# Kernel optimization log

Hardware: AMD Instinct MI355X
Metric: run time of the kernel (lower is better)

## Reference

```python
import jax, jax.numpy as jnp
import numpy as np

B, DIM, L, H, W = 4, 128, 256, 8, 8
N = L * H * W
D_INNER, D_STATE, D_CONV, DT_RANK = 128, 8, 4, 8


def _ln(x, w, b, eps=1e-5):
    m = x.mean(-1, keepdims=True)
    v = ((x - m) ** 2).mean(-1, keepdims=True)
    return (x - m) * jax.lax.rsqrt(v + eps) * w + b


def _mamba_fusion(x, z_in, p, i):
    # x, z_in: (B, N, DIM). x drives the SSM; z_in provides the cross-modal gate.
    u = x @ p['Wx'][i]                                    # (B, N, D_INNER)
    z = z_in @ p['Wz'][i]                                 # (B, N, D_INNER)
    # causal depthwise conv1d along tokens, kernel D_CONV (torch pad=k-1 then truncate)
    up = jnp.pad(u, ((0, 0), (D_CONV - 1, 0), (0, 0)))
    w = p['conv_w'][i]                                    # (D_INNER, D_CONV)
    uc = sum(up[:, k:k + u.shape[1], :] * w[:, k] for k in range(D_CONV)) + p['conv_b'][i]
    uc = jax.nn.silu(uc)
    x_dbl = uc @ p['Wxproj'][i]                           # (B, N, DT_RANK + 2*D_STATE)
    dt_r, Bm, Cm = jnp.split(x_dbl, [DT_RANK, DT_RANK + D_STATE], axis=-1)
    dt = jax.nn.softplus(dt_r @ p['Wdt'][i] + p['bdt'][i])  # (B, N, D_INNER)
    A = -jnp.exp(p['A_log'][i])                           # (D_INNER, D_STATE)
    dA = jnp.exp(dt[..., None] * A)                       # (B, N, D_INNER, D_STATE)
    dBu = dt[..., None] * Bm[:, :, None, :] * uc[..., None]

    def step(h, inp):
        dA_t, dBu_t, C_t = inp
        h = dA_t * h + dBu_t                              # (B, D_INNER, D_STATE)
        return h, jnp.einsum('bds,bs->bd', h, C_t)

    h0 = jnp.zeros((u.shape[0], D_INNER, D_STATE), u.dtype)
    _, ys = jax.lax.scan(step, h0, (dA.swapaxes(0, 1), dBu.swapaxes(0, 1), Cm.swapaxes(0, 1)))
    y = ys.swapaxes(0, 1) + p['Dp'][i] * uc
    y = y * jax.nn.silu(z)
    return y @ p['Wout_m'][i] + p['bout_m'][i]


def _cross_block(in0, in1, p, i):
    skip = in0
    a = _ln(in0, p['ln0_w'][i], p['ln0_b'][i])
    b = _ln(in1, p['ln1_w'][i], p['ln1_b'][i])
    return skip + _mamba_fusion(a, b, p, i)


def setup_inputs() -> dict:
    key = jax.random.key(0)
    ks = jax.random.split(key, 16)
    s_in = 1.0 / np.sqrt(DIM)
    s_di = 1.0 / np.sqrt(D_INNER)
    inp = {
        'front': jax.random.normal(ks[0], (B, DIM, L, H, W), jnp.float32),
        'back': jax.random.normal(ks[1], (B, DIM, L, H, W), jnp.float32),
        'ln0_w': jnp.ones((2, DIM), jnp.float32),
        'ln0_b': jnp.zeros((2, DIM), jnp.float32),
        'ln1_w': jnp.ones((2, DIM), jnp.float32),
        'ln1_b': jnp.zeros((2, DIM), jnp.float32),
        'Wx': jax.random.normal(ks[2], (2, DIM, D_INNER), jnp.float32) * s_in,
        'Wz': jax.random.normal(ks[3], (2, DIM, D_INNER), jnp.float32) * s_in,
        'conv_w': jax.random.normal(ks[4], (2, D_INNER, D_CONV), jnp.float32) * 0.5,
        'conv_b': jnp.zeros((2, D_INNER), jnp.float32),
        'Wxproj': jax.random.normal(ks[5], (2, D_INNER, DT_RANK + 2 * D_STATE), jnp.float32) * s_di,
        'Wdt': jax.random.normal(ks[6], (2, DT_RANK, D_INNER), jnp.float32) * (1.0 / np.sqrt(DT_RANK)),
        'bdt': jnp.full((2, D_INNER), -4.6, jnp.float32),  # softplus^-1(~0.01)
        'A_log': jnp.broadcast_to(jnp.log(jnp.arange(1, D_STATE + 1, dtype=jnp.float32)), (2, D_INNER, D_STATE)).copy(),
        'Dp': jnp.ones((2, D_INNER), jnp.float32),
        'Wout_m': jax.random.normal(ks[7], (2, D_INNER, DIM), jnp.float32) * s_di,
        'bout_m': jnp.zeros((2, DIM), jnp.float32),
        'Wout': jax.random.normal(ks[8], (DIM, DIM), jnp.float32) * s_in,
        'bout': jnp.zeros((DIM,), jnp.float32),
    }
    return inp


def reference(front, back, ln0_w, ln0_b, ln1_w, ln1_b, Wx, Wz, conv_w, conv_b,
              Wxproj, Wdt, bdt, A_log, Dp, Wout_m, bout_m, Wout, bout):
    p = dict(ln0_w=ln0_w, ln0_b=ln0_b, ln1_w=ln1_w, ln1_b=ln1_b, Wx=Wx, Wz=Wz,
             conv_w=conv_w, conv_b=conv_b, Wxproj=Wxproj, Wdt=Wdt, bdt=bdt,
             A_log=A_log, Dp=Dp, Wout_m=Wout_m, bout_m=bout_m)
    ff = front.reshape(B, DIM, N).swapaxes(1, 2)          # (B, N, DIM)
    bf = back.reshape(B, DIM, N).swapaxes(1, 2)
    f_fus = _cross_block(ff, bf, p, 0)
    b_fus = _cross_block(bf, ff, p, 1)
    fusion = ((f_fus + b_fus) * 0.5) @ Wout + bout
    return fusion.swapaxes(1, 2).reshape(B, DIM, L, H, W)
```

## Files before the change

### kernel.cpp

```cpp
#include <hip/hip_runtime.h>
#include <hip/hip_fp16.h>

#define DEV static __device__ __forceinline__

typedef short s16x8 __attribute__((ext_vector_type(8)));
typedef float f32x4 __attribute__((ext_vector_type(4)));
typedef unsigned short u16;

DEV float b2f(u16 u){ return __uint_as_float(((unsigned int)u) << 16); }
DEV u16 f2b(float f){
  unsigned int x = __float_as_uint(f);
  x += 0x7fffu + ((x >> 16) & 1u);
  return (u16)(x >> 16);
}
DEV u16 f2h(float f){ __half h = __float2half(f); u16 u; __builtin_memcpy(&u, &h, 2); return u; }
DEV float h2f(u16 u){ __half h; __builtin_memcpy(&h, &u, 2); return __half2float(h); }
DEV float silu_f(float x){ return x * __builtin_amdgcn_rcpf(1.f + __expf(-x)); }
DEV float softplus_f(float x){ return (x > 15.f) ? x : __logf(1.f + __expf(x)); }
DEV bool detf32(const void* lnw){ return *(const unsigned int*)lnw == 0x3F800000u; }
DEV float ldin(const void* p, long long i, bool f){
  return f ? ((const float*)p)[i] : b2f(((const u16*)p)[i]);
}

static constexpr int BATCH = 4;
static constexpr int NSEQ  = 16384;
static constexpr int RTOT  = BATCH * NSEQ;
static constexpr int GCH   = 256;
static constexpr int DIRSZ = BATCH*GCH*128*8;

DEV int swz(int row, int col){ return (row << 7) + (col ^ ((row & 7) << 3)); }

__global__ __launch_bounds__(256) void k_setup(
                        const void* ln0w, const void* ln0b, const void* ln1w, const void* ln1b,
                        const void* Wx, const void* Wz, const void* Wxp, const void* Wdt,
                        const void* bdt, const void* Alog, const void* convw, const void* convb,
                        const void* Dpr, const void* Woutm, const void* boutm,
                        const void* Wout, const void* bout,
                        u16* Wuz, u16* WdtBC, u16* Wcat, u16* WoutT,
                        float* buz, float* bdtf, float* bcat, float* boutf,
                        float* Aexp, float* convwF, float* convbF, float* DpF)
{
  bool f = detf32(ln0w);
  int tid = blockIdx.x * 256 + threadIdx.x;
  int gs  = gridDim.x * 256;
  for (int idx = tid; idx < 2*256*128; idx += gs){
    int d = idx >> 15; int n = (idx >> 7) & 255; int k = idx & 127;
    float wv;
    if (n < 128) wv = ldin(ln0w, d*128+k, f) * ldin(Wx, (long long)(d*128+k)*128 + n, f);
    else         wv = ldin(ln1w, (1-d)*128+k, f) * ldin(Wz, (long long)((1-d)*128+k)*128 + (n-128), f);
    Wuz[idx] = f2b(wv);
  }
  for (int idx = tid; idx < 2*256; idx += gs){
    int d = idx >> 8; int n = idx & 255;
    float s = 0.f;
    if (n < 128){
      for (int k = 0; k < 128; ++k)
        s += ldin(ln0b, d*128+k, f) * ldin(Wx, (long long)(d*128+k)*128 + n, f);
    } else {
      for (int k = 0; k < 128; ++k)
        s += ldin(ln1b, (1-d)*128+k, f) * ldin(Wz, (long long)((1-d)*128+k)*128 + (n-128), f);
    }
    buz[idx] = s;
  }
  for (int idx = tid; idx < 2*128; idx += gs)
    bdtf[idx] = ldin(bdt, idx, f);
  for (int idx = tid; idx < 2*144*128; idx += gs){
    int i = idx / (144*128); int rem = idx % (144*128); int n = rem >> 7; int k = rem & 127;
    if (n < 128){
      float s = 0.f;
      for (int j = 0; j < 8; ++j)
        s += ldin(Wxp, (long long)(i*128+k)*24 + j, f) * ldin(Wdt, (long long)(i*8+j)*128 + n, f);
      WdtBC[idx] = f2b(s);
    } else {
      WdtBC[idx] = f2b(ldin(Wxp, (long long)(i*128+k)*24 + (n - 120), f));
    }
  }
  for (int idx = tid; idx < 128*256; idx += gs){
    int n = idx >> 8; int k = idx & 255;
    Wcat[idx] = f2b(ldin(Woutm, (long long)k*128 + n, f));
  }
  for (int idx = tid; idx < 128*128; idx += gs){
    int n = idx >> 7, k = idx & 127;
    WoutT[idx] = f2b(ldin(Wout, (long long)k*128 + n, f));
  }
  for (int idx = tid; idx < 128; idx += gs){
    bcat[idx]  = ldin(boutm, idx, f) + ldin(boutm, 128 + idx, f);
    boutf[idx] = ldin(bout, idx, f);
  }
  for (int idx = tid; idx < 2*128*8; idx += gs)
    Aexp[idx] = -expf(ldin(Alog, idx, f));
  for (int idx = tid; idx < 2*128*4; idx += gs)
    convwF[idx] = ldin(convw, idx, f);
  for (int idx = tid; idx < 2*128; idx += gs){
    convbF[idx] = ldin(convb, idx, f);
    DpF[idx]   = ldin(Dpr, idx, f);
  }
}

__global__ __launch_bounds__(256) void k_ln(const void* front, const void* back, const void* ln0w,
                                            u16* xf, u16* xb, u16* sfbh)
{
  bool fF = detf32(ln0w);
  __shared__ u16 Af[64][130];
  __shared__ u16 Ab[64][130];
  __shared__ float Mf[64], Rf[64], Mb[64], Rb[64];
  int tid = threadIdx.x;
  long long r0 = (long long)blockIdx.x * 64;
  int b  = (int)(r0 >> 14);
  int n0 = (int)(r0 & 16383);
  if (fF){
    const float* fp = (const float*)front;
    const float* bp = (const float*)back;
    for (int it = 0; it < 8; ++it){
      int d = it*16 + (tid >> 4);
      int t = (tid & 15) * 4;
      long long gi = ((long long)(b*128 + d))*NSEQ + n0 + t;
      float4 vf = *(const float4*)&fp[gi];
      float4 vb = *(const float4*)&bp[gi];
      Af[t+0][d] = f2b(vf.x); Af[t+1][d] = f2b(vf.y);
      Af[t+2][d] = f2b(vf.z); Af[t+3][d] = f2b(vf.w);
      Ab[t+0][d] = f2b(vb.x); Ab[t+1][d] = f2b(vb.y);
      Ab[t+2][d] = f2b(vb.z); Ab[t+3][d] = f2b(vb.w);
    }
  } else {
    const u16* fp = (const u16*)front;
    const u16* bp = (const u16*)back;
    for (int it = 0; it < 4; ++it){
      int d = it*32 + (tid >> 3);
      int t = (tid & 7) * 8;
      long long gi = ((long long)(b*128 + d))*NSEQ + n0 + t;
      uint4 vf = *(const uint4*)&fp[gi];
      uint4 vb = *(const uint4*)&bp[gi];
      Af[t+0][d] = (u16)vf.x; Af[t+1][d] = (u16)(vf.x>>16);
      Af[t+2][d] = (u16)vf.y; Af[t+3][d] = (u16)(vf.y>>16);
      Af[t+4][d] = (u16)vf.z; Af[t+5][d] = (u16)(vf.z>>16);
      Af[t+6][d] = (u16)vf.w; Af[t+7][d] = (u16)(vf.w>>16);
      Ab[t+0][d] = (u16)vb.x; Ab[t+1][d] = (u16)(vb.x>>16);
      Ab[t+2][d] = (u16)vb.y; Ab[t+3][d] = (u16)(vb.y>>16);
      Ab[t+4][d] = (u16)vb.z; Ab[t+5][d] = (u16)(vb.z>>16);
      Ab[t+6][d] = (u16)vb.w; Ab[t+7][d] = (u16)(vb.w>>16);
    }
  }
  __syncthreads();
  {
    int t = tid >> 2, sub = tid & 3;
    float s = 0.f, ss = 0.f, s2 = 0.f, ss2 = 0.f;
    for (int k = 0; k < 32; ++k){
      float v = b2f(Af[t][sub*32 + k]); s  += v; ss  += v*v;
      float w = b2f(Ab[t][sub*32 + k]); s2 += w; ss2 += w*w;
    }
    for (int m = 1; m < 4; m <<= 1){
      s  += __shfl_xor(s,  m, 64); ss  += __shfl_xor(ss,  m, 64);
      s2 += __shfl_xor(s2, m, 64); ss2 += __shfl_xor(ss2, m, 64);
    }
    if (sub == 0){
      float mf = s  * (1.f/128.f); float vf = ss  * (1.f/128.f) - mf*mf;
      Mf[t] = mf; Rf[t] = rsqrtf(vf + 1e-5f);
      float mb = s2 * (1.f/128.f); float vb = ss2 * (1.f/128.f) - mb*mb;
      Mb[t] = mb; Rb[t] = rsqrtf(vb + 1e-5f);
    }
  }
  __syncthreads();
  for (int it = 0; it < 8; ++it){
    int t = it*8 + (tid >> 5);
    int c = (tid & 31) * 4;
    float mf = Mf[t], rf = Rf[t], mb = Mb[t], rb = Rb[t];
    float f0 = b2f(Af[t][c+0]), f1 = b2f(Af[t][c+1]), f2 = b2f(Af[t][c+2]), f3 = b2f(Af[t][c+3]);
    float g0 = b2f(Ab[t][c+0]), g1 = b2f(Ab[t][c+1]), g2 = b2f(Ab[t][c+2]), g3 = b2f(Ab[t][c+3]);
    ushort4 xo, zo, so;
    xo.x = f2b((f0-mf)*rf); xo.y = f2b((f1-mf)*rf); xo.z = f2b((f2-mf)*rf); xo.w = f2b((f3-mf)*rf);
    zo.x = f2b((g0-mb)*rb); zo.y = f2b((g1-mb)*rb); zo.z = f2b((g2-mb)*rb); zo.w = f2b((g3-mb)*rb);
    so.x = f2b(f0+g0); so.y = f2b(f1+g1); so.z = f2b(f2+g2); so.w = f2b(f3+g3);
    long long o = (r0 + t)*128 + c;
    *(ushort4*)&xf[o] = xo;
    *(ushort4*)&xb[o] = zo;
    *(ushort4*)&sfbh[o] = so;
  }
}

__global__ __launch_bounds__(256, 4) void k_guz(const u16* __restrict__ xf,
                                             const u16* __restrict__ xb,
                                             const u16* __restrict__ Wuz,
                                             const float* __restrict__ buz,
                                             u16* __restrict__ u0, u16* __restrict__ u1,
                                             u16* __restrict__ z0, u16* __restrict__ z1)
{
  int dir = blockIdx.y;
  const u16* A = dir ? xb : xf;
  const u16* Wt = Wuz + dir*256*128;
  const float* bias = buz + dir*256;
  u16* outU = dir ? u1 : u0;
  u16* outZ = dir ? z0 : z1;
  __shared__ __align__(16) u16 Wl[256*64];
  __shared__ __align__(16) u16 Al[64*64];
  int tid = threadIdx.x;
  long long r0 = (long long)blockIdx.x * 64;
  int w = tid >> 6, lane = tid & 63;
  int q = lane >> 4, m = lane & 15;
  f32x4 acc[16];
  #pragma unroll
  for (int ct = 0; ct < 16; ++ct) acc[ct] = (f32x4){0.f,0.f,0.f,0.f};
  for (int kp = 0; kp < 2; ++kp){
    if (kp) __syncthreads();
    for (int ci = tid; ci < 256*8; ci += 256){
      int n = ci >> 3, c8 = ci & 7;
      *(uint4*)&Wl[(n << 6) + ((c8 ^ (n & 7)) << 3)] = *(const uint4*)&Wt[n*128 + kp*64 + c8*8];
    }
    for (int ci = tid; ci < 64*8; ci += 256){
      int rl = ci >> 3, c8 = ci & 7;
      *(uint4*)&Al[(rl << 6) + ((c8 ^ (rl & 7)) << 3)] = *(const uint4*)&A[(r0 + rl)*128 + kp*64 + c8*8];
    }
    __syncthreads();
    #pragma unroll
    for (int kt = 0; kt < 2; ++kt){
      int sc = ((kt*4 + q) ^ (m & 7)) << 3;
      s16x8 af = *(const s16x8*)&Al[((w*16 + m) << 6) + sc];
      #pragma unroll
      for (int ct = 0; ct < 16; ++ct){
        s16x8 bf = *(const s16x8*)&Wl[((ct*16 + m) << 6) + sc];
        acc[ct] = __builtin_amdgcn_mfma_f32_16x16x32_bf16(af, bf, acc[ct], 0, 0, 0);
      }
    }
  }
  #pragma unroll
  for (int ct = 0; ct < 16; ++ct){
    int col = ct*16 + m;
    #pragma unroll
    for (int i = 0; i < 4; ++i){
      long long r = r0 + w*16 + q*4 + i;
      float v = acc[ct][i] + bias[col];
      if (col < 128) outU[r*128 + col] = f2b(v);
      else           outZ[r*128 + (col - 128)] = f2b(silu_f(v));
    }
  }
}

__global__ __launch_bounds__(256, 3) void k_cps(const u16* __restrict__ u0p,
                                             const u16* __restrict__ u1p,
                                             const float* __restrict__ convwF,
                                             const float* __restrict__ convbF,
                                             const u16* __restrict__ WdtBC,
                                             const float* __restrict__ bdtf,
                                             const float* __restrict__ Aexp,
                                             const float* __restrict__ DpF,
                                             u16* __restrict__ yl0, u16* __restrict__ yl1,
                                             u16* __restrict__ Eg,
                                             float* __restrict__ BCg,
                                             float* __restrict__ P, float* __restrict__ Q)
{
  __shared__ __align__(16) u16 AlF[64*128];
  __shared__ __align__(16) u16 WlF[144*128];
  int dir = blockIdx.y;
  const u16* u = dir ? u1p : u0p;
  const u16* Wt = WdtBC + dir*18432;
  const float* bias = bdtf + dir*128;
  float* BC = BCg + (long long)dir*RTOT*16;
  int tid = threadIdx.x;
  long long r0 = (long long)blockIdx.x * 64;
  int b  = (int)(r0 >> 14);
  int n0 = (int)(r0 & 16383);
  for (int ci = tid; ci < 144*16; ci += 256){
    int n = ci >> 4, c8 = ci & 15;
    *(uint4*)&WlF[(n << 7) + ((c8 ^ (n & 7)) << 3)] = *(const uint4*)&Wt[n*128 + c8*8];
  }
  {
    int c = tid & 127, h = tid >> 7;
    const float* wp = &convwF[(dir*128 + c)*4];
    float w0 = wp[0], w1 = wp[1], w2 = wp[2], w3 = wp[3];
    float cb = convbF[dir*128 + c];
    int t0 = h*32;
    const u16* up = u + (long long)b*NSEQ*128 + c;
    int nbase = n0 + t0;
    float win0 = (nbase-3 >= 0) ? b2f(up[(long long)(nbase-3)*128]) : 0.f;
    float win1 = (nbase-2 >= 0) ? b2f(up[(long long)(nbase-2)*128]) : 0.f;
    float win2 = (nbase-1 >= 0) ? b2f(up[(long long)(nbase-1)*128]) : 0.f;
    #pragma unroll
    for (int t = 0; t < 32; ++t){
      float cur = b2f(up[(long long)(nbase + t)*128]);
      float a = win0*w0 + win1*w1 + win2*w2 + cur*w3 + cb;
      AlF[swz(t0 + t, c)] = f2b(silu_f(a));
      win0 = win1; win1 = win2; win2 = cur;
    }
  }
  __syncthreads();
  int w = tid >> 6, lane = tid & 63;
  int q = lane >> 4, m = lane & 15;
  f32x4 acc[9];
  #pragma unroll
  for (int ct = 0; ct < 9; ++ct) acc[ct] = (f32x4){0.f,0.f,0.f,0.f};
  #pragma unroll
  for (int kt = 0; kt < 4; ++kt){
    int sc = (kt*32 + q*8) ^ ((m & 7) << 3);
    s16x8 af = *(const s16x8*)&AlF[((w*16 + m) << 7) + sc];
    #pragma unroll
    for (int ct = 0; ct < 9; ++ct){
      s16x8 bf = *(const s16x8*)&WlF[((ct*16 + m) << 7) + sc];
      acc[ct] = __builtin_amdgcn_mfma_f32_16x16x32_bf16(af, bf, acc[ct], 0, 0, 0);
    }
  }
  __syncthreads();
  u16* Dl = WlF;
  float* BCl = (float*)&WlF[64*128];
  #pragma unroll
  for (int ct = 0; ct < 9; ++ct){
    int col = ct*16 + m;
    #pragma unroll
    for (int i = 0; i < 4; ++i){
      int rl = w*16 + q*4 + i;
      long long r = r0 + rl;
      float v = acc[ct][i];
      if (col < 128){
        Dl[swz(rl, col)] = f2b(softplus_f(v + bias[col]));
      } else {
        BCl[rl*16 + (col - 128)] = v;
        if (col >= 136) BC[r*16 + (col - 128)] = v;
      }
    }
  }
  __syncthreads();
  if (tid < 128){
    int c = tid;
    int g = (int)(r0 & 16383) >> 6;
    float Ac[8], H[8];
    bool fast = true;
    #pragma unroll
    for (int s = 0; s < 8; ++s){
      Ac[s] = Aexp[(dir*128 + c)*8 + s];
      fast = fast && (fabsf(Ac[s] + (float)(s + 1)) < 2e-4f);
      H[s] = 0.f;
    }
    float dpc = DpF[dir*128 + c];
    u16* ylArr = dir ? yl1 : yl0;
    u16* EArr  = Eg + (size_t)dir*((size_t)RTOT*128);
    long long sb = r0*128 + c;
    float PE = 1.f, sd = 0.f;
    if (fast){
      for (int t = 0; t < 64; ++t){
        int ce = swz(t, c);
        float d  = b2f(Dl[ce]);
        float uu = b2f(AlF[ce]);
        float du = d * uu;
        float E1 = __expf(-d);
        PE *= E1;
        float E2=E1*E1, E3=E2*E1, E4=E2*E2;
        float E5=E4*E1, E6=E4*E2, E7=E4*E3, E8=E4*E4;
        float4 b0 = *(const float4*)&BCl[t*16];
        float4 b1 = *(const float4*)&BCl[t*16 + 4];
        float4 c0 = *(const float4*)&BCl[t*16 + 8];
        float4 c1 = *(const float4*)&BCl[t*16 + 12];
        H[0]=E1*H[0]+du*b0.x; H[1]=E2*H[1]+du*b0.y;
        H[2]=E3*H[2]+du*b0.z; H[3]=E4*H[3]+du*b0.w;
        H[4]=E5*H[4]+du*b1.x; H[5]=E6*H[5]+du*b1.y;
        H[6]=E7*H[6]+du*b1.z; H[7]=E8*H[7]+du*b1.w;
        float y = H[0]*c0.x + H[1]*c0.y + H[2]*c0.z + H[3]*c0.w
                + H[4]*c1.x + H[5]*c1.y + H[6]*c1.z + H[7]*c1.w;
        ylArr[sb + (long long)t*128] = f2b(y + dpc*uu);
        EArr [sb + (long long)t*128] = f2h(PE);
      }
    } else {
      for (int t = 0; t < 64; ++t){
        int ce = swz(t, c);
        float d  = b2f(Dl[ce]);
        float uu = b2f(AlF[ce]);
        float du = d * uu;
        sd += d;
        float y = 0.f;
        #pragma unroll
        for (int s = 0; s < 8; ++s){
          float dA = __expf(d * Ac[s]);
          H[s] = dA*H[s] + du*BCl[t*16 + s];
          y += H[s]*BCl[t*16 + 8 + s];
        }
        ylArr[sb + (long long)t*128] = f2b(y + dpc*uu);
        EArr [sb + (long long)t*128] = f2b(sd);
      }
    }
    long long o = (long long)dir*DIRSZ + (((long long)b*GCH + g)*128 + c)*8;
    float Pr[8];
    if (fast){
      float P2=PE*PE, P3=P2*PE, P4=P2*P2;
      Pr[0]=PE; Pr[1]=P2; Pr[2]=P3; Pr[3]=P4;
      Pr[4]=P4*PE; Pr[5]=P4*P2; Pr[6]=P4*P3; Pr[7]=P4*P4;
    } else {
      #pragma unroll
      for (int s = 0; s < 8; ++s) Pr[s] = __expf(sd * Ac[s]);
    }
    *(float4*)&P[o]     = make_float4(Pr[0],Pr[1],Pr[2],Pr[3]);
    *(float4*)&P[o + 4] = make_float4(Pr[4],Pr[5],Pr[6],Pr[7]);
    *(float4*)&Q[o]     = make_float4(H[0],H[1],H[2],H[3]);
    *(float4*)&Q[o + 4] = make_float4(H[4],H[5],H[6],H[7]);
  }
}

__global__ __launch_bounds__(64) void k_scan2(const float* __restrict__ P,
                                              const float* __restrict__ Q,
                                              float* __restrict__ hinit)
{
  int idx = blockIdx.x*64 + threadIdx.x;
  int dir = idx >> 12;
  int rem = idx & 4095;
  int b  = rem >> 10;
  int cs = rem & 1023;
  long long base = (long long)dir*DIRSZ + (long long)b*GCH*1024 + cs;
  float h = 0.f;
  for (int g = 0; g < GCH; g += 8){
    long long o = base + (long long)g*1024;
    float p[8], qv[8];
    #pragma unroll
    for (int j = 0; j < 8; ++j){ p[j] = P[o + j*1024]; qv[j] = Q[o + j*1024]; }
    #pragma unroll
    for (int j = 0; j < 8; ++j){
      hinit[o + j*1024] = h;
      h = p[j]*h + qv[j];
    }
  }
}

__global__ __launch_bounds__(256, 3) void k_tail(const u16* __restrict__ yl0,
                                              const u16* __restrict__ yl1,
                                              const u16* __restrict__ Eg,
                                              const float* __restrict__ BCg,
                                              const float* __restrict__ hinit,
                                              const u16* __restrict__ z0p,
                                              const u16* __restrict__ z1p,
                                              const float* __restrict__ Aexp,
                                              const u16* __restrict__ Wcat,
                                              const float* __restrict__ bcat,
                                              const u16* __restrict__ sfbh,
                                              const u16* __restrict__ WoutT,
                                              const float* __restrict__ boutf,
                                              void* outp, const void* dflag)
{
  __shared__ u16 Wl[128][136];
  __shared__ u16 Al[64][136];
  int tid = threadIdx.x;
  long long r0 = (long long)blockIdx.x * 64;
  int bb = (int)(r0 >> 14);
  int g  = ((int)(r0 & 16383)) >> 6;
  int w = tid >> 6, lane = tid & 63;
  int q = lane >> 4, m = lane & 15;
  int pc = tid & 127, rh = tid >> 7;
  f32x4 acc[8];
  #pragma unroll
  for (int ct = 0; ct < 8; ++ct) acc[ct] = (f32x4){0.f,0.f,0.f,0.f};
  for (int kp = 0; kp < 2; ++kp){
    if (kp) __syncthreads();
    for (int ci = tid; ci < 128*16; ci += 256){
      int n = ci >> 4, c8 = ci & 15;
      *(uint4*)&Wl[n][c8*8] = *(const uint4*)&Wcat[n*256 + kp*128 + c8*8];
    }
    {
      const u16* ylv = kp ? yl1 : yl0;
      const u16* Ev  = Eg + (size_t)kp*((size_t)RTOT*128);
      const u16* zs  = kp ? z1p : z0p;
      const float* BCd = BCg + (size_t)kp*((size_t)RTOT*16);
      float h[8];
      {
        long long ho = (long long)kp*DIRSZ + (((long long)bb*GCH + g)*128 + pc)*8;
        float4 h0v = *(const float4*)&hinit[ho];
        float4 h1v = *(const float4*)&hinit[ho + 4];
        h[0]=h0v.x; h[1]=h0v.y; h[2]=h0v.z; h[3]=h0v.w;
        h[4]=h1v.x; h[5]=h1v.y; h[6]=h1v.z; h[7]=h1v.w;
      }
      float Ac[8]; bool fastc = true;
      #pragma unroll
      for (int s = 0; s < 8; ++s){
        Ac[s] = Aexp[(kp*128 + pc)*8 + s];
        fastc = fastc && (fabsf(Ac[s] + (float)(s + 1)) < 2e-4f);
      }
      long long sb = (r0 + rh*32)*128 + pc;
      if (fastc){
        for (int i = 0; i < 32; ++i){
          int t = rh*32 + i;
          long long r = r0 + t;
          float4 c0 = *(const float4*)&BCd[r*16 + 8];
          float4 c1 = *(const float4*)&BCd[r*16 + 12];
          float yl = b2f(ylv[sb + (long long)i*128]);
          float E  = h2f(Ev [sb + (long long)i*128]);
          float corr =          h[7]*c1.w;
          corr = corr*E + h[6]*c1.z;
          corr = corr*E + h[5]*c1.y;
          corr = corr*E + h[4]*c1.x;
          corr = corr*E + h[3]*c0.w;
          corr = corr*E + h[2]*c0.z;
          corr = corr*E + h[1]*c0.y;
          corr = corr*E + h[0]*c0.x;
          corr *= E;
          float zz = b2f(zs[sb + (long long)i*128]);
          Al[t][pc] = f2b((yl + corr)*zz);
        }
      } else {
        for (int i = 0; i < 32; ++i){
          int t = rh*32 + i;
          long long r = r0 + t;
          float yl = b2f(ylv[sb + (long long)i*128]);
          float cd = b2f(Ev [sb + (long long)i*128]);
          float corr = 0.f;
          #pragma unroll
          for (int s = 0; s < 8; ++s)
            corr += h[s]*BCd[r*16 + 8 + s]*__expf(cd*Ac[s]);
          float zz = b2f(zs[sb + (long long)i*128]);
          Al[t][pc] = f2b((yl + corr)*zz);
        }
      }
    }
    __syncthreads();
    #pragma unroll
    for (int kt = 0; kt < 4; ++kt){
      s16x8 af = *(const s16x8*)&Al[w*16 + m][kt*32 + q*8];
      #pragma unroll
      for (int ct = 0; ct < 8; ++ct){
        s16x8 bf = *(const s16x8*)&Wl[ct*16 + m][kt*32 + q*8];
        acc[ct] = __builtin_amdgcn_mfma_f32_16x16x32_bf16(af, bf, acc[ct], 0, 0, 0);
      }
    }
  }
  __syncthreads();
  #pragma unroll
  for (int ct = 0; ct < 8; ++ct){
    int col = ct*16 + m;
    #pragma unroll
    for (int i = 0; i < 4; ++i){
      int rl = w*16 + q*4 + i;
      long long r = r0 + rl;
      Al[rl][col] = f2b(acc[ct][i] + bcat[col] + b2f(sfbh[r*128 + col]));
    }
  }
  for (int ci = tid; ci < 128*16; ci += 256){
    int n = ci >> 4, c8 = ci & 15;
    *(uint4*)&Wl[n][c8*8] = *(const uint4*)&WoutT[n*128 + c8*8];
  }
  __syncthreads();
  f32x4 acc2[8];
  #pragma unroll
  for (int ct = 0; ct < 8; ++ct) acc2[ct] = (f32x4){0.f,0.f,0.f,0.f};
  #pragma unroll
  for (int kt = 0; kt < 4; ++kt){
    s16x8 af = *(const s16x8*)&Al[w*16 + m][kt*32 + q*8];
    #pragma unroll
    for (int ct = 0; ct < 8; ++ct){
      s16x8 bf = *(const s16x8*)&Wl[ct*16 + m][kt*32 + q*8];
      acc2[ct] = __builtin_amdgcn_mfma_f32_16x16x32_bf16(af, bf, acc2[ct], 0, 0, 0);
    }
  }
  __syncthreads();
  u16* Tl = &Wl[0][0];
  #pragma unroll
  for (int ct = 0; ct < 8; ++ct){
    int col = ct*16 + m;
    #pragma unroll
    for (int i = 0; i < 4; ++i){
      int rl = w*16 + q*4 + i;
      Tl[col*68 + rl] = f2b(0.5f*acc2[ct][i] + boutf[col]);
    }
  }
  __syncthreads();
  long long b = r0 >> 14; long long tok0 = r0 & 16383;
  bool fo = detf32(dflag);
  if (fo){
    float* of = (float*)outp;
    for (int idx = tid; idx < 128*16; idx += 256){
      int n = idx >> 4; int t0 = (idx & 15)*4;
      float4 v;
      v.x = b2f(Tl[n*68 + t0+0]); v.y = b2f(Tl[n*68 + t0+1]);
      v.z = b2f(Tl[n*68 + t0+2]); v.w = b2f(Tl[n*68 + t0+3]);
      *(float4*)&of[(((long long)(b*128 + n)) << 14) + tok0 + t0] = v;
    }
  } else {
    u16* ob = (u16*)outp;
    for (int idx = tid; idx < 128*16; idx += 256){
      int n = idx >> 4; int t0 = (idx & 15)*4;
      ushort4 v;
      v.x = Tl[n*68 + t0+0]; v.y = Tl[n*68 + t0+1];
      v.z = Tl[n*68 + t0+2]; v.w = Tl[n*68 + t0+3];
      *(ushort4*)&ob[(((long long)(b*128 + n)) << 14) + tok0 + t0] = v;
    }
  }
}

extern "C" void kernel_launch(void* const* d_in, const int* in_sizes, int n_in,
                              void* d_out, int out_size, void* d_ws, size_t ws_size,
                              hipStream_t stream)
{
  (void)in_sizes; (void)n_in; (void)out_size; (void)ws_size;
  const void* front = d_in[0];
  const void* back  = d_in[1];
  const void* ln0w  = d_in[2];
  const void* ln0b  = d_in[3];
  const void* ln1w  = d_in[4];
  const void* ln1b  = d_in[5];
  const void* Wx    = d_in[6];
  const void* Wz    = d_in[7];
  const void* convw = d_in[8];
  const void* convb = d_in[9];
  const void* Wxp   = d_in[10];
  const void* Wdt   = d_in[11];
  const void* bdt   = d_in[12];
  const void* Alog  = d_in[13];
  const void* Dpr   = d_in[14];
  const void* Woutm = d_in[15];
  const void* boutm = d_in[16];
  const void* Wout  = d_in[17];
  const void* bout  = d_in[18];

  char* p = (char*)d_ws;
  auto alloc = [&](size_t bytes) -> void* {
    void* q = (void*)p; p += (bytes + 255) & ~(size_t)255; return q;
  };
  u16*   xf    = (u16*)  alloc((size_t)RTOT*128*2);
  u16*   xb    = (u16*)  alloc((size_t)RTOT*128*2);
  u16*   sfbh  = (u16*)  alloc((size_t)RTOT*128*2);
  u16*   u0    = (u16*)  alloc((size_t)RTOT*128*2);
  u16*   u1    = (u16*)  alloc((size_t)RTOT*128*2);
  u16*   z0    = (u16*)  alloc((size_t)RTOT*128*2);
  u16*   z1    = (u16*)  alloc((size_t)RTOT*128*2);
  float* BC    = (float*)alloc((size_t)2*RTOT*16*4);
  float* Pb    = (float*)alloc((size_t)2*DIRSZ*4);
  float* Qb    = (float*)alloc((size_t)2*DIRSZ*4);
  float* hin   = (float*)alloc((size_t)2*DIRSZ*4);
  u16*   Eg    = (u16*)  alloc((size_t)RTOT*256*2);
  u16*   Wuz   = (u16*)  alloc(2*256*128*2);
  u16*   WdtBC = (u16*)  alloc(2*144*128*2);
  u16*   Wcat  = (u16*)  alloc(128*256*2);
  u16*   WoutT = (u16*)  alloc(128*128*2);
  float* buz   = (float*)alloc(2*256*4);
  float* bdtf  = (float*)alloc(2*128*4);
  float* bcat  = (float*)alloc(128*4);
  float* boutf = (float*)alloc(128*4);
  float* Aexp  = (float*)alloc(2*128*8*4);
  float* convwF= (float*)alloc(2*128*4*4);
  float* convbF= (float*)alloc(2*128*4);
  float* DpF   = (float*)alloc(2*128*4);

  k_setup<<<128,256,0,stream>>>(ln0w,ln0b,ln1w,ln1b,Wx,Wz,Wxp,Wdt,bdt,Alog,convw,convb,Dpr,
                                Woutm,boutm,Wout,bout,
                                Wuz,WdtBC,Wcat,WoutT,buz,bdtf,bcat,boutf,Aexp,
                                convwF,convbF,DpF);
  k_ln<<<RTOT/64,256,0,stream>>>(front,back,ln0w,xf,xb,sfbh);

  dim3 g2(RTOT/64, 2);
  k_guz<<<g2,256,0,stream>>>(xf, xb, Wuz, buz, u0, u1, z0, z1);
  k_cps<<<g2,256,0,stream>>>(u0, u1, convwF, convbF, WdtBC, bdtf, Aexp, DpF,
                             xf, xb, Eg, BC, Pb, Qb);
  k_scan2<<<128,64,0,stream>>>(Pb, Qb, hin);
  k_tail<<<RTOT/64,256,0,stream>>>(xf, xb, Eg, BC, hin, z0, z1, Aexp,
                                   Wcat, bcat, sfbh, WoutT, boutf, d_out, ln0w);
}
```

Before: 342.8 us.

## Split SSM chunk scan state across all threads and pack y/E into one word

The intra-chunk scan in k_cps previously ran on only 128 of 256 threads, each carrying all 8 state elements. It now uses all 256 threads, each handling 4 of the 8 states for one channel, and combines the partial outputs with a cross-half shuffle. The local y and decay values are also packed into one 32-bit word per element, so k_tail does one load instead of two. The fallback path now writes exp(-sd) in fp16 when a channel is fast but the wave is not, which changes the encoding that path relies on. It also adds shuffle overhead and leaves half the lanes idle during stores.

```diff
diff --git a/kernel.cpp b/kernel.cpp
--- a/kernel.cpp
+++ b/kernel.cpp
@@ -6,6 +6,7 @@
 typedef short s16x8 __attribute__((ext_vector_type(8)));
 typedef float f32x4 __attribute__((ext_vector_type(4)));
 typedef unsigned short u16;
+typedef unsigned int u32;
 
 DEV float b2f(u16 u){ return __uint_as_float(((unsigned int)u) << 16); }
 DEV u16 f2b(float f){
@@ -243,8 +244,7 @@
                                              const float* __restrict__ bdtf,
                                              const float* __restrict__ Aexp,
                                              const float* __restrict__ DpF,
-                                             u16* __restrict__ yl0, u16* __restrict__ yl1,
-                                             u16* __restrict__ Eg,
+                                             u32* __restrict__ ylEg,
                                              float* __restrict__ BCg,
                                              float* __restrict__ P, float* __restrict__ Q)
 {
@@ -318,23 +318,26 @@
     }
   }
   __syncthreads();
-  if (tid < 128){
-    int c = tid;
+  {
+    int li = lane & 31, sh = lane >> 5;
+    int c = w*32 + li;
     int g = (int)(r0 & 16383) >> 6;
-    float Ac[8], H[8];
-    bool fast = true;
-    #pragma unroll
-    for (int s = 0; s < 8; ++s){
-      Ac[s] = Aexp[(dir*128 + c)*8 + s];
-      fast = fast && (fabsf(Ac[s] + (float)(s + 1)) < 2e-4f);
-      H[s] = 0.f;
-    }
+    int base = sh*4;
+    float Ac[4];
+    bool f4 = true;
+    #pragma unroll
+    for (int j = 0; j < 4; ++j){
+      Ac[j] = Aexp[(dir*128 + c)*8 + base + j];
+      f4 = f4 && (fabsf(Ac[j] + (float)(base + j + 1)) < 2e-4f);
+    }
+    bool cfast = f4 && (__shfl_xor((int)f4, 32, 64) != 0);
+    bool fastw = (__ballot(cfast) == ~0ull);
     float dpc = DpF[dir*128 + c];
-    u16* ylArr = dir ? yl1 : yl0;
-    u16* EArr  = Eg + (size_t)dir*((size_t)RTOT*128);
+    u32* ylE = ylEg + (size_t)dir*((size_t)RTOT*128);
     long long sb = r0*128 + c;
+    float H0=0.f, H1=0.f, H2=0.f, H3=0.f;
     float PE = 1.f, sd = 0.f;
-    if (fast){
+    if (fastw){
       for (int t = 0; t < 64; ++t){
         int ce = swz(t, c);
         float d  = b2f(Dl[ce]);
@@ -342,20 +345,17 @@
         float du = d * uu;
         float E1 = __expf(-d);
         PE *= E1;
-        float E2=E1*E1, E3=E2*E1, E4=E2*E2;
-        float E5=E4*E1, E6=E4*E2, E7=E4*E3, E8=E4*E4;
-        float4 b0 = *(const float4*)&BCl[t*16];
-        float4 b1 = *(const float4*)&BCl[t*16 + 4];
-        float4 c0 = *(const float4*)&BCl[t*16 + 8];
-        float4 c1 = *(const float4*)&BCl[t*16 + 12];
-        H[0]=E1*H[0]+du*b0.x; H[1]=E2*H[1]+du*b0.y;
-        H[2]=E3*H[2]+du*b0.z; H[3]=E4*H[3]+du*b0.w;
-        H[4]=E5*H[4]+du*b1.x; H[5]=E6*H[5]+du*b1.y;
-        H[6]=E7*H[6]+du*b1.z; H[7]=E8*H[7]+du*b1.w;
-        float y = H[0]*c0.x + H[1]*c0.y + H[2]*c0.z + H[3]*c0.w
-                + H[4]*c1.x + H[5]*c1.y + H[6]*c1.z + H[7]*c1.w;
-        ylArr[sb + (long long)t*128] = f2b(y + dpc*uu);
-        EArr [sb + (long long)t*128] = f2h(PE);
+        float E2 = E1*E1, E3 = E2*E1, E4 = E2*E2;
+        float M  = sh ? E4 : 1.f;
+        float dA0 = M*E1, dA1 = M*E2, dA2 = M*E3, dA3 = M*E4;
+        float4 bb = *(const float4*)&BCl[t*16 + base];
+        float4 cc = *(const float4*)&BCl[t*16 + 8 + base];
+        H0 = dA0*H0 + du*bb.x; H1 = dA1*H1 + du*bb.y;
+        H2 = dA2*H2 + du*bb.z; H3 = dA3*H3 + du*bb.w;
+        float yp = H0*cc.x + H1*cc.y + H2*cc.z + H3*cc.w;
+        float yo = yp + __shfl_xor(yp, 32, 64);
+        if (sh == 0)
+          ylE[sb + (long long)t*128] = ((u32)f2h(PE) << 16) | (u32)f2b(yo + dpc*uu);
       }
     } else {
       for (int t = 0; t < 64; ++t){
@@ -364,31 +364,33 @@
         float uu = b2f(AlF[ce]);
         float du = d * uu;
         sd += d;
-        float y = 0.f;
         #pragma unroll
-        for (int s = 0; s < 8; ++s){
-          float dA = __expf(d * Ac[s]);
-          H[s] = dA*H[s] + du*BCl[t*16 + s];
-          y += H[s]*BCl[t*16 + 8 + s];
+        for (int j = 0; j < 4; ++j){
+          float dA = __expf(d * Ac[j]);
+          float* Hj = (j==0)?&H0:(j==1)?&H1:(j==2)?&H2:&H3;
+          *Hj = dA*(*Hj) + du*BCl[t*16 + base + j];
         }
-        ylArr[sb + (long long)t*128] = f2b(y + dpc*uu);
-        EArr [sb + (long long)t*128] = f2b(sd);
-      }
-    }
-    long long o = (long long)dir*DIRSZ + (((long long)b*GCH + g)*128 + c)*8;
-    float Pr[8];
-    if (fast){
-      float P2=PE*PE, P3=P2*PE, P4=P2*P2;
-      Pr[0]=PE; Pr[1]=P2; Pr[2]=P3; Pr[3]=P4;
-      Pr[4]=P4*PE; Pr[5]=P4*P2; Pr[6]=P4*P3; Pr[7]=P4*P4;
+        float yp = H0*BCl[t*16 + 8 + base + 0] + H1*BCl[t*16 + 8 + base + 1]
+                 + H2*BCl[t*16 + 8 + base + 2] + H3*BCl[t*16 + 8 + base + 3];
+        float yo = yp + __shfl_xor(yp, 32, 64);
+        if (sh == 0){
+          u16 eh = cfast ? f2h(__expf(-sd)) : f2b(sd);
+          ylE[sb + (long long)t*128] = ((u32)eh << 16) | (u32)f2b(yo + dpc*uu);
+        }
+      }
+    }
+    float Pr0, Pr1, Pr2, Pr3;
+    if (fastw){
+      float P2 = PE*PE, P3 = P2*PE, P4 = P2*P2;
+      float Pm = sh ? P4 : 1.f;
+      Pr0 = Pm*PE; Pr1 = Pm*P2; Pr2 = Pm*P3; Pr3 = Pm*P4;
     } else {
-      #pragma unroll
-      for (int s = 0; s < 8; ++s) Pr[s] = __expf(sd * Ac[s]);
-    }
-    *(float4*)&P[o]     = make_float4(Pr[0],Pr[1],Pr[2],Pr[3]);
-    *(float4*)&P[o + 4] = make_float4(Pr[4],Pr[5],Pr[6],Pr[7]);
-    *(float4*)&Q[o]     = make_float4(H[0],H[1],H[2],H[3]);
-    *(float4*)&Q[o + 4] = make_float4(H[4],H[5],H[6],H[7]);
+      Pr0 = __expf(sd*Ac[0]); Pr1 = __expf(sd*Ac[1]);
+      Pr2 = __expf(sd*Ac[2]); Pr3 = __expf(sd*Ac[3]);
+    }
+    long long o = (long long)dir*DIRSZ + (((long long)b*GCH + g)*128 + c)*8 + base;
+    *(float4*)&P[o] = make_float4(Pr0,Pr1,Pr2,Pr3);
+    *(float4*)&Q[o] = make_float4(H0,H1,H2,H3);
   }
 }
 
@@ -416,9 +418,7 @@
   }
 }
 
-__global__ __launch_bounds__(256, 3) void k_tail(const u16* __restrict__ yl0,
-                                              const u16* __restrict__ yl1,
-                                              const u16* __restrict__ Eg,
+__global__ __launch_bounds__(256, 3) void k_tail(const u32* __restrict__ ylEg,
                                               const float* __restrict__ BCg,
                                               const float* __restrict__ hinit,
                                               const u16* __restrict__ z0p,
@@ -450,8 +450,7 @@
       *(uint4*)&Wl[n][c8*8] = *(const uint4*)&Wcat[n*256 + kp*128 + c8*8];
     }
     {
-      const u16* ylv = kp ? yl1 : yl0;
-      const u16* Ev  = Eg + (size_t)kp*((size_t)RTOT*128);
+      const u32* ylE = ylEg + (size_t)kp*((size_t)RTOT*128);
       const u16* zs  = kp ? z1p : z0p;
       const float* BCd = BCg + (size_t)kp*((size_t)RTOT*16);
       float h[8];
@@ -475,8 +474,9 @@
           long long r = r0 + t;
           float4 c0 = *(const float4*)&BCd[r*16 + 8];
           float4 c1 = *(const float4*)&BCd[r*16 + 12];
-          float yl = b2f(ylv[sb + (long long)i*128]);
-          float E  = h2f(Ev [sb + (long long)i*128]);
+          u32 ve = ylE[sb + (long long)i*128];
+          float yl = b2f((u16)(ve & 0xffffu));
+          float E  = h2f((u16)(ve >> 16));
           float corr =          h[7]*c1.w;
           corr = corr*E + h[6]*c1.z;
           corr = corr*E + h[5]*c1.y;
@@ -493,8 +493,9 @@
         for (int i = 0; i < 32; ++i){
           int t = rh*32 + i;
           long long r = r0 + t;
-          float yl = b2f(ylv[sb + (long long)i*128]);
-          float cd = b2f(Ev [sb + (long long)i*128]);
+          u32 ve = ylE[sb + (long long)i*128];
+          float yl = b2f((u16)(ve & 0xffffu));
+          float cd = b2f((u16)(ve >> 16));
           float corr = 0.f;
           #pragma unroll
           for (int s = 0; s < 8; ++s)
@@ -618,7 +619,7 @@
   float* Pb    = (float*)alloc((size_t)2*DIRSZ*4);
   float* Qb    = (float*)alloc((size_t)2*DIRSZ*4);
   float* hin   = (float*)alloc((size_t)2*DIRSZ*4);
-  u16*   Eg    = (u16*)  alloc((size_t)RTOT*256*2);
+  u32*   ylE   = (u32*)  alloc((size_t)2*RTOT*128*4);
   u16*   Wuz   = (u16*)  alloc(2*256*128*2);
   u16*   WdtBC = (u16*)  alloc(2*144*128*2);
   u16*   Wcat  = (u16*)  alloc(128*256*2);
@@ -641,8 +642,8 @@
   dim3 g2(RTOT/64, 2);
   k_guz<<<g2,256,0,stream>>>(xf, xb, Wuz, buz, u0, u1, z0, z1);
   k_cps<<<g2,256,0,stream>>>(u0, u1, convwF, convbF, WdtBC, bdtf, Aexp, DpF,
-                             xf, xb, Eg, BC, Pb, Qb);
+                             ylE, BC, Pb, Qb);
   k_scan2<<<128,64,0,stream>>>(Pb, Qb, hin);
-  k_tail<<<RTOT/64,256,0,stream>>>(xf, xb, Eg, BC, hin, z0, z1, Aexp,
+  k_tail<<<RTOT/64,256,0,stream>>>(ylE, BC, hin, z0, z1, Aexp,
                                    Wcat, bcat, sfbh, WoutT, boutf, d_out, ln0w);
 }
```

After: 337.4 us. Within noise of the previous version (-1.6%).
